# Kernel tuning notes

Hardware: AMD Instinct MI355X
Metric: run time of the kernel (lower is better)

The kernel has to match this reference:

```python
import jax, jax.numpy as jnp
import numpy as np

D, NH, NL, NP, DFF = 256, 8, 4, 4, 1024
DH = D // NH
# 4-level FPN of a 1024x1024 image at strides 8/16/32/64 (H, W per level)
SHAPES = np.array([[128, 128], [64, 64], [32, 32], [16, 16]], dtype=np.int32)


def setup_inputs() -> dict:
    ks = jax.random.split(jax.random.key(0), 16)
    B, Lq = 4, 900
    sizes = SHAPES[:, 0] * SHAPES[:, 1]
    Lin = int(sizes.sum())
    starts = np.concatenate([[0], np.cumsum(sizes)[:-1]]).astype(np.int32)
    s = 0.02  # small init so softmax/LN stay well-conditioned

    def w(k, shape):
        return jax.random.normal(k, shape, jnp.float32) * s

    return {
        "tgt": jax.random.normal(ks[0], (Lq, B, D), jnp.float32),
        "tgt_reference_points": jax.random.uniform(ks[1], (Lq, B, NL, 2), jnp.float32),
        "memory": jax.random.normal(ks[2], (Lin, B, D), jnp.float32),
        "W_off": w(ks[3], (NH * NL * NP * 2, D)), "b_off": w(ks[4], (NH * NL * NP * 2,)),
        "W_attn": w(ks[5], (NH * NL * NP, D)), "b_attn": w(ks[6], (NH * NL * NP,)),
        "W_val": w(ks[7], (D, D)), "b_val": w(ks[8], (D,)),
        "W_out": w(ks[9], (D, D)), "b_out": w(ks[10], (D,)),
        "ln1_g": jnp.ones((D,), jnp.float32), "ln1_b": jnp.zeros((D,), jnp.float32),
        "W1": w(ks[11], (DFF, D)), "b1": w(ks[12], (DFF,)),
        "W2": w(ks[13], (D, DFF)), "b2": w(ks[14], (D,)),
        "ln3_g": jnp.ones((D,), jnp.float32), "ln3_b": jnp.zeros((D,), jnp.float32),
        "memory_spatial_shapes": jnp.asarray(SHAPES),
        "memory_level_start_index": jnp.asarray(starts),
        "memory_key_padding_mask": jnp.zeros((B, Lin), jnp.bool_),
    }


def _ln(x, g, b, eps=1e-5):
    mu = x.mean(-1, keepdims=True)
    var = ((x - mu) ** 2).mean(-1, keepdims=True)
    return (x - mu) * jax.lax.rsqrt(var + eps) * g + b


def _bilinear(vl, loc, H, W):
    # vl: (B, NH, H*W, DH); loc: (B, Lq, NH, NP, 2) normalized to [0,1]
    # matches torch grid_sample(mode='bilinear', padding_mode='zeros', align_corners=False)
    B, Lq, nh, P, _ = loc.shape
    x = loc[..., 0] * W - 0.5
    y = loc[..., 1] * H - 0.5
    x0f = jnp.floor(x)
    y0f = jnp.floor(y)
    x0 = x0f.astype(jnp.int32)
    y0 = y0f.astype(jnp.int32)
    wx1 = x - x0f
    wy1 = y - y0f

    def tap(xi, yi, w):
        valid = (xi >= 0) & (xi < W) & (yi >= 0) & (yi < H)
        idx = jnp.clip(yi, 0, H - 1) * W + jnp.clip(xi, 0, W - 1)
        idx = idx.transpose(0, 2, 1, 3).reshape(B, nh, Lq * P)
        ww = (w * valid).transpose(0, 2, 1, 3).reshape(B, nh, Lq * P)
        vals = jnp.take_along_axis(vl, idx[..., None], axis=2)  # (B,NH,Lq*P,DH)
        return vals * ww[..., None]

    acc = (tap(x0, y0, (1 - wx1) * (1 - wy1)) + tap(x0 + 1, y0, wx1 * (1 - wy1))
           + tap(x0, y0 + 1, (1 - wx1) * wy1) + tap(x0 + 1, y0 + 1, wx1 * wy1))
    return acc.reshape(B, nh, Lq, P, DH)


def _msda(q, ref, value, shapes_np, W_off, b_off, W_attn, b_attn, W_out, b_out):
    # q: (B,Lq,D), ref: (B,Lq,NL,2), value: (B,Lin,NH,DH)
    B, Lq, _ = q.shape
    off = (q @ W_off.T + b_off).reshape(B, Lq, NH, NL, NP, 2)
    a = jax.nn.softmax((q @ W_attn.T + b_attn).reshape(B, Lq, NH, NL * NP), axis=-1)
    a = a.reshape(B, Lq, NH, NL, NP)
    norm = jnp.asarray(shapes_np[:, ::-1].copy(), jnp.float32)  # (NL, 2) as (W, H)
    loc = ref[:, :, None, :, None, :] + off / norm[None, None, None, :, None, :]
    sizes = [int(h) * int(w) for h, w in shapes_np]
    starts = np.concatenate([[0], np.cumsum(sizes)[:-1]])
    v = value.transpose(0, 2, 1, 3)  # (B, NH, Lin, DH)
    out = jnp.zeros((B, NH, Lq, DH), q.dtype)
    for l, (H, W) in enumerate(shapes_np):
        vl = v[:, :, int(starts[l]):int(starts[l]) + sizes[l], :]
        sampled = _bilinear(vl, loc[:, :, :, l], int(H), int(W))  # (B,NH,Lq,NP,DH)
        wl = a[:, :, :, l].transpose(0, 2, 1, 3)  # (B,NH,Lq,NP)
        out = out + (sampled * wl[..., None]).sum(3)
    out = out.transpose(0, 2, 1, 3).reshape(B, Lq, D)
    return out @ W_out.T + b_out


def reference(tgt, tgt_reference_points, memory, W_off, b_off, W_attn, b_attn,
              W_val, b_val, W_out, b_out, ln1_g, ln1_b, W1, b1, W2, b2, ln3_g, ln3_b,
              memory_spatial_shapes, memory_level_start_index, memory_key_padding_mask):
    shapes_np = np.asarray(memory_spatial_shapes)  # static level metadata
    q = tgt.transpose(1, 0, 2)                      # (B, Lq, D)
    ref = tgt_reference_points.transpose(1, 0, 2, 3)
    mem = memory.transpose(1, 0, 2)                 # (B, Lin, D)
    B, Lin, _ = mem.shape
    value = mem @ W_val.T + b_val
    value = jnp.where(memory_key_padding_mask[..., None], 0.0, value)
    value = value.reshape(B, Lin, NH, DH)
    ca = _msda(q, ref, value, shapes_np, W_off, b_off, W_attn, b_attn, W_out, b_out)
    # residual + LN (dropout is identity in eval)
    t = _ln(tgt + ca.transpose(1, 0, 2), ln1_g, ln1_b)
    # FFN
    t2 = jax.nn.relu(t @ W1.T + b1) @ W2.T + b2
    return _ln(t + t2, ln3_g, ln3_b)
```

## Files before the change

kernel.cpp:

```cpp
#include <hip/hip_runtime.h>
#include <hip/hip_bf16.h>

#define B_   4
#define LQ_  900
#define D_   256
#define NH_  8
#define DH_  32
#define NL_  4
#define NP_  4
#define DFF_ 1024
#define LIN_ 21760
#define MQ_  (LQ_*B_)
#define MV_  (LIN_*B_)
#define VALBLKS (MV_/32)

typedef __attribute__((ext_vector_type(8))) short bh8;
typedef __attribute__((ext_vector_type(4))) float f32x4;

__device__ __forceinline__ short bf16b(float f) {
    __hip_bfloat16 h = __float2bfloat16(f);
    return *reinterpret_cast<short*>(&h);
}

__device__ __forceinline__ void gload_lds16(const void* g, void* l) {
    __builtin_amdgcn_global_load_lds(
        (const __attribute__((address_space(1))) unsigned int*)g,
        (__attribute__((address_space(3))) unsigned int*)l, 16, 0, 0);
}

__device__ __forceinline__ bh8 af_from_f32(const float* p) {
    float4 v0 = *reinterpret_cast<const float4*>(p);
    float4 v1 = *reinterpret_cast<const float4*>(p + 4);
    return (bh8){ bf16b(v0.x), bf16b(v0.y), bf16b(v0.z), bf16b(v0.w),
                  bf16b(v1.x), bf16b(v1.y), bf16b(v1.z), bf16b(v1.w) };
}

__global__ __launch_bounds__(256)
void wprep_k(const float* __restrict__ Woff, const float* __restrict__ Wattn,
             const float* __restrict__ Wout, const float* __restrict__ W1,
             const float* __restrict__ W2, const float* __restrict__ Wval,
             unsigned char* __restrict__ qkvimg, unsigned char* __restrict__ outimg,
             unsigned char* __restrict__ w1img, unsigned char* __restrict__ w2img,
             unsigned char* __restrict__ valimg)
{
    const int cid = blockIdx.x*256 + threadIdx.x;
    const float* W; unsigned char* img; int KQ, c;
    if      (cid < 8192)  { W=Woff;  img=qkvimg;           KQ=8;  c=cid;       }
    else if (cid < 12288) { W=Wattn; img=qkvimg + 131072;  KQ=8;  c=cid-8192;  }
    else if (cid < 20480) { W=Wout;  img=outimg;           KQ=8;  c=cid-12288; }
    else if (cid < 53248) { W=W1;    img=w1img;            KQ=8;  c=cid-20480; }
    else if (cid < 86016) { W=W2;    img=w2img;            KQ=32; c=cid-53248; }
    else                  { W=Wval;  img=valimg;           KQ=8;  c=cid-86016; }
    const int K   = KQ*32;
    const int n16 = c & 15, g = (c>>4)&3, t = c>>6;
    const int kq  = t & (KQ-1);
    const int ntile = t >> ((KQ==8) ? 3 : 5);
    const int n = ntile*16 + n16, k0 = kq*32 + g*8;
    float4 v0 = *reinterpret_cast<const float4*>(&W[(size_t)n*K + k0]);
    float4 v1 = *reinterpret_cast<const float4*>(&W[(size_t)n*K + k0 + 4]);
    union { short s[8]; uint4 u; } pk;
    pk.s[0]=bf16b(v0.x); pk.s[1]=bf16b(v0.y); pk.s[2]=bf16b(v0.z); pk.s[3]=bf16b(v0.w);
    pk.s[4]=bf16b(v1.x); pk.s[5]=bf16b(v1.y); pk.s[6]=bf16b(v1.z); pk.s[7]=bf16b(v1.w);
    *reinterpret_cast<uint4*>(img + (size_t)(ntile*KQ + kq)*1024 + (g*16+n16)*16) = pk.u;
}

__global__ __launch_bounds__(256, 4)
void valqkv_k(const float* __restrict__ A, const unsigned char* __restrict__ Wimg,
              const float* __restrict__ bias, unsigned short* __restrict__ C,
              const unsigned char* __restrict__ mask,
              const float* __restrict__ tgt, const unsigned char* __restrict__ Qimg,
              const float* __restrict__ b_off, const float* __restrict__ b_attn,
              float* __restrict__ Yoff, float* __restrict__ Yattn)
{
    __shared__ __align__(16) unsigned char Al[32768];

    const int tid  = threadIdx.x;
    const int lane = tid & 63;

    if (blockIdx.x < VALBLKS) {
        const int wc   = tid >> 6;
        const int m0   = blockIdx.x * 32;
        const int r16  = lane & 15;
        const int g    = lane >> 4;

        const unsigned char* Abyte = (const unsigned char*)A;
        const unsigned char* wlane = Wimg + lane*16;

        const int a_row = (tid >> 3) & 31;
        const int a_x   = (tid & 7) * 16;
        const size_t a_src_row = (size_t)(m0 + a_row) * 1024 + (a_x ^ ((a_row & 7) << 4));
        const int a_dst = tid * 16;

#define ISSUE_A(KQ) gload_lds16(Abyte + a_src_row + (KQ)*128, (char*)Al + (KQ)*4096 + a_dst)
#define ISSUE_W(KQ, SLOT)                                                              \
    do { _Pragma("unroll")                                                             \
        for (int i_ = 0; i_ < 4; ++i_)                                                 \
            bfr[SLOT][i_] = *reinterpret_cast<const bh8*>(                             \
                wlane + (size_t)((wc*4 + i_)*8 + (KQ))*1024);                          \
    } while (0)

        bh8 bfr[3][4];

        ISSUE_A(0);
        ISSUE_W(0, 0);
        ISSUE_W(1, 1);
        ISSUE_A(1);
        ISSUE_A(2);

        f32x4 acc[2][4];
        #pragma unroll
        for (int i = 0; i < 2; ++i)
            #pragma unroll
            for (int j = 0; j < 4; ++j) acc[i][j] = (f32x4){0.f,0.f,0.f,0.f};

        #pragma unroll
        for (int kq = 0; kq < 8; ++kq) {
            if (kq < 6)      asm volatile("s_waitcnt vmcnt(6)" ::: "memory");
            else if (kq == 6) asm volatile("s_waitcnt vmcnt(5)" ::: "memory");
            else              asm volatile("s_waitcnt vmcnt(0)" ::: "memory");
            __builtin_amdgcn_s_barrier();

            bh8 af[2];
            #pragma unroll
            for (int mf = 0; mf < 2; ++mf) {
                const int row = mf*16 + r16;
                const int swz = (row & 7) << 4;
                const char* base = (const char*)Al + kq*4096 + row*128;
                float4 v0 = *reinterpret_cast<const float4*>(base + ((g*32     ) ^ swz));
                float4 v1 = *reinterpret_cast<const float4*>(base + ((g*32 + 16) ^ swz));
                af[mf] = (bh8){ bf16b(v0.x), bf16b(v0.y), bf16b(v0.z), bf16b(v0.w),
                                bf16b(v1.x), bf16b(v1.y), bf16b(v1.z), bf16b(v1.w) };
            }

            if (kq == 0) { ISSUE_W(2, 2); ISSUE_A(3); }
            if (kq == 1) { ISSUE_W(3, 0); ISSUE_A(4); }
            if (kq == 2) { ISSUE_W(4, 1); ISSUE_A(5); }
            if (kq == 3) { ISSUE_W(5, 2); ISSUE_A(6); }
            if (kq == 4) { ISSUE_W(6, 0); ISSUE_A(7); }
            if (kq == 5) { ISSUE_W(7, 1); }

            #pragma unroll
            for (int mf = 0; mf < 2; ++mf)
                #pragma unroll
                for (int i = 0; i < 4; ++i)
                    acc[mf][i] = __builtin_amdgcn_mfma_f32_16x16x32_bf16(af[mf], bfr[kq % 3][i], acc[mf][i], 0, 0, 0);
        }
#undef ISSUE_A
#undef ISSUE_W

        float bv[4];
        #pragma unroll
        for (int i = 0; i < 4; ++i) bv[i] = bias[wc*64 + i*16 + r16];

        #pragma unroll
        for (int mf = 0; mf < 2; ++mf) {
            #pragma unroll
            for (int r = 0; r < 4; ++r) {
                const int gm = m0 + mf*16 + g*4 + r;
                const bool z = mask[(gm & 3)*LIN_ + (gm >> 2)] != 0;
                #pragma unroll
                for (int i = 0; i < 4; ++i) {
                    float v = acc[mf][i][r] + bv[i];
                    if (z) v = 0.f;
                    C[(size_t)gm*256 + wc*64 + i*16 + r16] = (unsigned short)bf16b(v);
                }
            }
        }
    } else {
        const int w   = tid >> 6;
        const int m16 = lane & 15, g = lane >> 4;
        const int m0  = (blockIdx.x - VALBLKS) * 16;

        bh8 af[8];
        #pragma unroll
        for (int kq = 0; kq < 8; ++kq)
            af[kq] = af_from_f32(&tgt[(size_t)(m0 + m16)*256 + kq*32 + g*8]);

        f32x4 acc[6];
        #pragma unroll
        for (int i = 0; i < 6; ++i) acc[i] = (f32x4){0.f,0.f,0.f,0.f};

        #pragma unroll
        for (int i = 0; i < 6; ++i) {
            const int nt = w*6 + i;
            #pragma unroll
            for (int kq = 0; kq < 8; ++kq) {
                bh8 bf = *reinterpret_cast<const bh8*>(Qimg + (size_t)(nt*8 + kq)*1024 + lane*16);
                acc[i] = __builtin_amdgcn_mfma_f32_16x16x32_bf16(af[kq], bf, acc[i], 0, 0, 0);
            }
        }

        #pragma unroll
        for (int i = 0; i < 6; ++i) {
            const int nt = w*6 + i;
            const int j  = nt*16 + m16;
            #pragma unroll
            for (int r = 0; r < 4; ++r) {
                const int m = m0 + g*4 + r;
                if (nt < 16) Yoff[(size_t)m*256 + j] = acc[i][r] + b_off[j];
                else         Yattn[(size_t)m*128 + (j-256)] = acc[i][r] + b_attn[j-256];
            }
        }
    }
}

__global__ __launch_bounds__(1024, 2)
void outffn_k(const float* __restrict__ Amsda, const unsigned char* __restrict__ Oimg,
              const float* __restrict__ b_out, const float* __restrict__ res,
              const float* __restrict__ l1g, const float* __restrict__ l1b,
              const unsigned char* __restrict__ W1img, const float* __restrict__ b1,
              const unsigned char* __restrict__ W2img, const float* __restrict__ b2,
              const float* __restrict__ l3g, const float* __restrict__ l3b,
              float* __restrict__ Yout)
{
    __shared__ float sln[16][256];
    __shared__ __align__(16) short hl[2][16*272];

    const int tid = threadIdx.x, lane = tid & 63, w = tid >> 6;
    const int m16 = lane & 15, g = lane >> 4;
    const int m0 = blockIdx.x * 16;

    {
        bh8 af[8];
        #pragma unroll
        for (int kq = 0; kq < 8; ++kq)
            af[kq] = af_from_f32(&Amsda[(size_t)(m0 + m16)*256 + kq*32 + g*8]);

        f32x4 acc = (f32x4){0.f,0.f,0.f,0.f};
        #pragma unroll
        for (int kq = 0; kq < 8; ++kq) {
            bh8 bf = *reinterpret_cast<const bh8*>(Oimg + (size_t)(w*8 + kq)*1024 + lane*16);
            acc = __builtin_amdgcn_mfma_f32_16x16x32_bf16(af[kq], bf, acc, 0, 0, 0);
        }

        const int j = w*16 + m16;
        #pragma unroll
        for (int r = 0; r < 4; ++r) {
            const int ml = g*4 + r;
            sln[ml][j] = acc[r] + b_out[j] + res[(size_t)(m0 + ml)*256 + j];
        }
    }
    __syncthreads();

    {
        const int row = w, l2 = lane;
        float v[4], s1 = 0.f, s2 = 0.f;
        #pragma unroll
        for (int c = 0; c < 4; ++c) {
            v[c] = sln[row][l2 + c*64];
            s1 += v[c]; s2 += v[c]*v[c];
        }
        #pragma unroll
        for (int o = 32; o >= 1; o >>= 1) {
            s1 += __shfl_xor(s1, o, 64);
            s2 += __shfl_xor(s2, o, 64);
        }
        const float mu  = s1 * (1.f/256.f);
        const float var = s2 * (1.f/256.f) - mu*mu;
        const float is  = rsqrtf(var + 1e-5f);
        #pragma unroll
        for (int c = 0; c < 4; ++c) {
            const int jj = l2 + c*64;
            sln[row][jj] = (v[c] - mu) * is * l1g[jj] + l1b[jj];
        }
    }
    __syncthreads();

    bh8 af1[8];
    #pragma unroll
    for (int kq = 0; kq < 8; ++kq)
        af1[kq] = af_from_f32(&sln[m16][kq*32 + g*8]);

    f32x4 yacc = (f32x4){0.f,0.f,0.f,0.f};

    int buf = 0;
    #pragma unroll
    for (int fc = 0; fc < 4; ++fc) {
        const int ftile_g = fc*16 + w;
        f32x4 hacc = (f32x4){0.f,0.f,0.f,0.f};
        #pragma unroll
        for (int kq = 0; kq < 8; ++kq) {
            bh8 bf = *reinterpret_cast<const bh8*>(W1img + (size_t)(ftile_g*8 + kq)*1024 + lane*16);
            hacc = __builtin_amdgcn_mfma_f32_16x16x32_bf16(af1[kq], bf, hacc, 0, 0, 0);
        }
        const float bb = b1[ftile_g*16 + m16];
        #pragma unroll
        for (int r = 0; r < 4; ++r) {
            const float v = fmaxf(hacc[r] + bb, 0.f);
            hl[buf][(g*4 + r)*272 + w*16 + m16] = bf16b(v);
        }
        __syncthreads();
        bh8 a2[8];
        #pragma unroll
        for (int kqf = 0; kqf < 8; ++kqf)
            a2[kqf] = *reinterpret_cast<const bh8*>((const char*)&hl[buf][0]
                + m16*544 + (kqf*32 + g*8)*2);
        #pragma unroll
        for (int kqf = 0; kqf < 8; ++kqf) {
            const int kq2 = fc*8 + kqf;
            bh8 bf = *reinterpret_cast<const bh8*>(W2img + (size_t)(w*32 + kq2)*1024 + lane*16);
            yacc = __builtin_amdgcn_mfma_f32_16x16x32_bf16(a2[kqf], bf, yacc, 0, 0, 0);
        }
        buf ^= 1;
    }

    {
        const int j = w*16 + m16;
        #pragma unroll
        for (int r = 0; r < 4; ++r) {
            const int ml = g*4 + r;
            sln[ml][j] = yacc[r] + b2[j] + sln[ml][j];
        }
    }
    __syncthreads();

    {
        const int row = w, l2 = lane;
        float v[4], s1 = 0.f, s2 = 0.f;
        #pragma unroll
        for (int c = 0; c < 4; ++c) {
            v[c] = sln[row][l2 + c*64];
            s1 += v[c]; s2 += v[c]*v[c];
        }
        #pragma unroll
        for (int o = 32; o >= 1; o >>= 1) {
            s1 += __shfl_xor(s1, o, 64);
            s2 += __shfl_xor(s2, o, 64);
        }
        const float mu  = s1 * (1.f/256.f);
        const float var = s2 * (1.f/256.f) - mu*mu;
        const float is  = rsqrtf(var + 1e-5f);
        #pragma unroll
        for (int c = 0; c < 4; ++c) {
            const int jj = l2 + c*64;
            Yout[(size_t)(m0 + row)*256 + jj] = (v[c] - mu) * is * l3g[jj] + l3b[jj];
        }
    }
}

__global__ __launch_bounds__(256)
void msda_k(const float* __restrict__ off,
            const float* __restrict__ attnlog,
            const float* __restrict__ refp,
            const __hip_bfloat16* __restrict__ value,
            float* __restrict__ out)
{
    const int hp = threadIdx.x >> 7;
    const int dd = threadIdx.x & 127;
    const int d0 = dd * 2;
    const int m  = blockIdx.x*2 + hp;
    const int b  = m & 3;
    const int h  = dd >> 4;

    __shared__ float s_off[2][256];
    __shared__ float s_al[2][128];
    __shared__ float s_ref[2][NL_*2];
    {
        const int t2 = threadIdx.x & 127;
        s_off[hp][t2]       = off[(size_t)m*256 + t2];
        s_off[hp][t2 + 128] = off[(size_t)m*256 + t2 + 128];
        if (t2 < 128) s_al[hp][t2] = attnlog[(size_t)m*128 + t2];
        if (t2 < NL_*2) s_ref[hp][t2] = refp[(size_t)m*(NL_*2) + t2];
    }
    __syncthreads();

    float mx = -1e30f;
    #pragma unroll
    for (int t = 0; t < 16; ++t) mx = fmaxf(mx, s_al[hp][h*16 + t]);
    float e[16], ssum = 0.f;
    #pragma unroll
    for (int t = 0; t < 16; ++t) { e[t] = __expf(s_al[hp][h*16 + t] - mx); ssum += e[t]; }
    const float inv = 1.f / ssum;

    const int HS[4] = {128, 64, 32, 16};
    const int ST[4] = {0, 16384, 20480, 21504};

    float acc0 = 0.f, acc1 = 0.f;
    #pragma unroll
    for (int l = 0; l < NL_; ++l) {
        const int H = HS[l], W = HS[l], st = ST[l];
        const float rx = s_ref[hp][l*2+0], ry = s_ref[hp][l*2+1];
        #pragma unroll
        for (int p = 0; p < NP_; ++p) {
            const int base = ((h*NL_ + l)*NP_ + p);
            const float a  = e[l*4 + p] * inv;
            const float ox = s_off[hp][base*2+0], oy = s_off[hp][base*2+1];
            const float x = rx*(float)W + ox - 0.5f;
            const float y = ry*(float)H + oy - 0.5f;
            const float x0f = floorf(x), y0f = floorf(y);
            const int x0 = (int)x0f, y0 = (int)y0f;
            const float wx1 = x - x0f, wy1 = y - y0f;
            const float wx0 = 1.f - wx1, wy0 = 1.f - wy1;
            #pragma unroll
            for (int t = 0; t < 4; ++t) {
                const int xi = x0 + (t & 1);
                const int yi = y0 + (t >> 1);
                const float wgt = (t==0 ? wx0*wy0 : t==1 ? wx1*wy0 : t==2 ? wx0*wy1 : wx1*wy1);
                if (xi >= 0 && xi < W && yi >= 0 && yi < H) {
                    const size_t idx = (size_t)(st + yi*W + xi);
                    const unsigned int v = *reinterpret_cast<const unsigned int*>(
                        &value[(idx*B_ + b)*D_ + d0]);
                    const float f0 = __uint_as_float(v << 16);
                    const float f1 = __uint_as_float(v & 0xffff0000u);
                    const float aw = a * wgt;
                    acc0 = fmaf(aw, f0, acc0);
                    acc1 = fmaf(aw, f1, acc1);
                }
            }
        }
    }
    float2 o2 = { acc0, acc1 };
    *reinterpret_cast<float2*>(&out[(size_t)m*256 + d0]) = o2;
}

extern "C" void kernel_launch(void* const* d_in, const int* in_sizes, int n_in,
                              void* d_out, int out_size, void* d_ws, size_t ws_size,
                              hipStream_t stream)
{
    const float* tgt    = (const float*)d_in[0];
    const float* refp   = (const float*)d_in[1];
    const float* mem    = (const float*)d_in[2];
    const float* W_off  = (const float*)d_in[3];
    const float* b_off  = (const float*)d_in[4];
    const float* W_attn = (const float*)d_in[5];
    const float* b_attn = (const float*)d_in[6];
    const float* W_val  = (const float*)d_in[7];
    const float* b_val  = (const float*)d_in[8];
    const float* W_out  = (const float*)d_in[9];
    const float* b_out  = (const float*)d_in[10];
    const float* ln1g   = (const float*)d_in[11];
    const float* ln1b   = (const float*)d_in[12];
    const float* W1     = (const float*)d_in[13];
    const float* b1     = (const float*)d_in[14];
    const float* W2     = (const float*)d_in[15];
    const float* b2     = (const float*)d_in[16];
    const float* ln3g   = (const float*)d_in[17];
    const float* ln3b   = (const float*)d_in[18];
    const unsigned char* mask = (const unsigned char*)d_in[21];
    float* out = (float*)d_out;

    char* p = (char*)d_ws;
    __hip_bfloat16* value = (__hip_bfloat16*)p; p += (size_t)MV_*D_*2;
    float* offb = (float*)p; p += (size_t)MQ_*256*4;
    float* attl = (float*)p; p += (size_t)MQ_*128*4;
    float* msda = (float*)p; p += (size_t)MQ_*256*4;
    unsigned char* qkvimg = (unsigned char*)p; p += 196608;
    unsigned char* outimg = (unsigned char*)p; p += 131072;
    unsigned char* w1img  = (unsigned char*)p; p += 524288;
    unsigned char* w2img  = (unsigned char*)p; p += 524288;
    unsigned char* valimg = (unsigned char*)p; p += 131072;
    (void)ws_size; (void)in_sizes; (void)n_in; (void)out_size;

    wprep_k<<<dim3(368), dim3(256), 0, stream>>>(W_off, W_attn, W_out, W1, W2, W_val,
                                                 qkvimg, outimg, w1img, w2img, valimg);
    valqkv_k<<<dim3(VALBLKS + MQ_/16), dim3(256), 0, stream>>>(
        mem, valimg, b_val, (unsigned short*)value, mask,
        tgt, qkvimg, b_off, b_attn, offb, attl);
    msda_k<<<dim3(MQ_/2), dim3(256), 0, stream>>>(offb, attl, refp, value, msda);
    outffn_k<<<dim3(MQ_/16), dim3(1024), 0, stream>>>(
        msda, outimg, b_out, tgt, ln1g, ln1b,
        w1img, b1, w2img, b2, ln3g, ln3b, out);
}
```

Before: 99.43 us.

## Fuse deformable-attention sampling into the output-projection/FFN kernel

The separate msda kernel is removed. Its bilinear sampling now runs at the start of outffn_k, where each of the 16 waves handles one query row and writes the sampled result into shared memory, so the fp32 msda buffer no longer round-trips through global memory and one launch is dropped. The cost is that the sampling now runs on only 225 blocks of 1024 threads, each thread doing two channel pairs in sequence. This lowers parallelism and latency hiding for the gather-heavy stage, and the extra shared memory (about 50KB) may cut occupancy.

```diff
diff --git a/kernel.cpp b/kernel.cpp
--- a/kernel.cpp
+++ b/kernel.cpp
@@ -205,26 +205,107 @@
 }
 
 __global__ __launch_bounds__(1024, 2)
-void outffn_k(const float* __restrict__ Amsda, const unsigned char* __restrict__ Oimg,
-              const float* __restrict__ b_out, const float* __restrict__ res,
+void outffn_k(const float* __restrict__ off, const float* __restrict__ attnlog,
+              const float* __restrict__ refp, const __hip_bfloat16* __restrict__ value,
+              const unsigned char* __restrict__ Oimg, const float* __restrict__ b_out,
+              const float* __restrict__ res,
               const float* __restrict__ l1g, const float* __restrict__ l1b,
               const unsigned char* __restrict__ W1img, const float* __restrict__ b1,
               const unsigned char* __restrict__ W2img, const float* __restrict__ b2,
               const float* __restrict__ l3g, const float* __restrict__ l3b,
               float* __restrict__ Yout)
 {
-    __shared__ float sln[16][256];
+    __shared__ float X[16][264];
+    __shared__ float off_l[16][256];
+    __shared__ float al_l[16][128];
+    __shared__ float ref_l[16][8];
     __shared__ __align__(16) short hl[2][16*272];
 
     const int tid = threadIdx.x, lane = tid & 63, w = tid >> 6;
     const int m16 = lane & 15, g = lane >> 4;
     const int m0 = blockIdx.x * 16;
 
+    #pragma unroll
+    for (int i = 0; i < 4; ++i) {
+        const int idx = tid + i*1024;
+        off_l[idx >> 8][idx & 255] = off[(size_t)(m0 + (idx >> 8))*256 + (idx & 255)];
+    }
+    #pragma unroll
+    for (int i = 0; i < 2; ++i) {
+        const int idx = tid + i*1024;
+        al_l[idx >> 7][idx & 127] = attnlog[(size_t)(m0 + (idx >> 7))*128 + (idx & 127)];
+    }
+    if (tid < 128) ref_l[tid >> 3][tid & 7] = refp[(size_t)(m0 + (tid >> 3))*8 + (tid & 7)];
+    __syncthreads();
+
+    {
+        const int row = w;
+        const int b = (m0 + row) & 3;
+        const int HS[4] = {128, 64, 32, 16};
+        const int ST[4] = {0, 16384, 20480, 21504};
+        float r0[2], r1[2];
+        #pragma unroll
+        for (int uu = 0; uu < 2; ++uu) {
+            const int u  = lane + uu*64;
+            const int d0 = u*2;
+            const int h  = u >> 4;
+            float mx = -1e30f;
+            #pragma unroll
+            for (int t = 0; t < 16; ++t) mx = fmaxf(mx, al_l[row][h*16 + t]);
+            float e[16], ssum = 0.f;
+            #pragma unroll
+            for (int t = 0; t < 16; ++t) { e[t] = __expf(al_l[row][h*16 + t] - mx); ssum += e[t]; }
+            const float inv = 1.f / ssum;
+            float a0 = 0.f, a1 = 0.f;
+            #pragma unroll
+            for (int l = 0; l < NL_; ++l) {
+                const int H = HS[l], Wd = HS[l], st = ST[l];
+                const float rx = ref_l[row][l*2+0], ry = ref_l[row][l*2+1];
+                #pragma unroll
+                for (int p = 0; p < NP_; ++p) {
+                    const int base = ((h*NL_ + l)*NP_ + p);
+                    const float a  = e[l*4 + p] * inv;
+                    const float ox = off_l[row][base*2+0], oy = off_l[row][base*2+1];
+                    const float x = rx*(float)Wd + ox - 0.5f;
+                    const float y = ry*(float)H + oy - 0.5f;
+                    const float x0f = floorf(x), y0f = floorf(y);
+                    const int x0 = (int)x0f, y0 = (int)y0f;
+                    const float wx1 = x - x0f, wy1 = y - y0f;
+                    const float wx0 = 1.f - wx1, wy0 = 1.f - wy1;
+                    #pragma unroll
+                    for (int t = 0; t < 4; ++t) {
+                        const int xi = x0 + (t & 1);
+                        const int yi = y0 + (t >> 1);
+                        const float wgt = (t==0 ? wx0*wy0 : t==1 ? wx1*wy0 : t==2 ? wx0*wy1 : wx1*wy1);
+                        if (xi >= 0 && xi < Wd && yi >= 0 && yi < H) {
+                            const size_t idx = (size_t)(st + yi*Wd + xi);
+                            const unsigned int v = *reinterpret_cast<const unsigned int*>(
+                                &value[(idx*B_ + b)*D_ + d0]);
+                            const float f0 = __uint_as_float(v << 16);
+                            const float f1 = __uint_as_float(v & 0xffff0000u);
+                            const float aw = a * wgt;
+                            a0 = fmaf(aw, f0, a0);
+                            a1 = fmaf(aw, f1, a1);
+                        }
+                    }
+                }
+            }
+            r0[uu] = a0; r1[uu] = a1;
+        }
+        #pragma unroll
+        for (int uu = 0; uu < 2; ++uu) {
+            const int d0 = (lane + uu*64)*2;
+            X[row][d0]   = r0[uu];
+            X[row][d0+1] = r1[uu];
+        }
+    }
+    __syncthreads();
+
     {
         bh8 af[8];
         #pragma unroll
         for (int kq = 0; kq < 8; ++kq)
-            af[kq] = af_from_f32(&Amsda[(size_t)(m0 + m16)*256 + kq*32 + g*8]);
+            af[kq] = af_from_f32(&X[m16][kq*32 + g*8]);
 
         f32x4 acc = (f32x4){0.f,0.f,0.f,0.f};
         #pragma unroll
@@ -232,22 +313,22 @@
             bh8 bf = *reinterpret_cast<const bh8*>(Oimg + (size_t)(w*8 + kq)*1024 + lane*16);
             acc = __builtin_amdgcn_mfma_f32_16x16x32_bf16(af[kq], bf, acc, 0, 0, 0);
         }
+        __syncthreads();
 
         const int j = w*16 + m16;
         #pragma unroll
         for (int r = 0; r < 4; ++r) {
             const int ml = g*4 + r;
-            sln[ml][j] = acc[r] + b_out[j] + res[(size_t)(m0 + ml)*256 + j];
+            X[ml][j] = acc[r] + b_out[j] + res[(size_t)(m0 + ml)*256 + j];
         }
     }
     __syncthreads();
 
     {
-        const int row = w, l2 = lane;
         float v[4], s1 = 0.f, s2 = 0.f;
         #pragma unroll
         for (int c = 0; c < 4; ++c) {
-            v[c] = sln[row][l2 + c*64];
+            v[c] = X[w][lane + c*64];
             s1 += v[c]; s2 += v[c]*v[c];
         }
         #pragma unroll
@@ -260,8 +341,8 @@
         const float is  = rsqrtf(var + 1e-5f);
         #pragma unroll
         for (int c = 0; c < 4; ++c) {
-            const int jj = l2 + c*64;
-            sln[row][jj] = (v[c] - mu) * is * l1g[jj] + l1b[jj];
+            const int jj = lane + c*64;
+            X[w][jj] = (v[c] - mu) * is * l1g[jj] + l1b[jj];
         }
     }
     __syncthreads();
@@ -269,7 +350,7 @@
     bh8 af1[8];
     #pragma unroll
     for (int kq = 0; kq < 8; ++kq)
-        af1[kq] = af_from_f32(&sln[m16][kq*32 + g*8]);
+        af1[kq] = af_from_f32(&X[m16][kq*32 + g*8]);
 
     f32x4 yacc = (f32x4){0.f,0.f,0.f,0.f};
 
@@ -309,17 +390,16 @@
         #pragma unroll
         for (int r = 0; r < 4; ++r) {
             const int ml = g*4 + r;
-            sln[ml][j] = yacc[r] + b2[j] + sln[ml][j];
+            X[ml][j] = yacc[r] + b2[j] + X[ml][j];
         }
     }
     __syncthreads();
 
     {
-        const int row = w, l2 = lane;
         float v[4], s1 = 0.f, s2 = 0.f;
         #pragma unroll
         for (int c = 0; c < 4; ++c) {
-            v[c] = sln[row][l2 + c*64];
+            v[c] = X[w][lane + c*64];
             s1 += v[c]; s2 += v[c]*v[c];
         }
         #pragma unroll
@@ -332,85 +412,10 @@
         const float is  = rsqrtf(var + 1e-5f);
         #pragma unroll
         for (int c = 0; c < 4; ++c) {
-            const int jj = l2 + c*64;
-            Yout[(size_t)(m0 + row)*256 + jj] = (v[c] - mu) * is * l3g[jj] + l3b[jj];
-        }
-    }
-}
-
-__global__ __launch_bounds__(256)
-void msda_k(const float* __restrict__ off,
-            const float* __restrict__ attnlog,
-            const float* __restrict__ refp,
-            const __hip_bfloat16* __restrict__ value,
-            float* __restrict__ out)
-{
-    const int hp = threadIdx.x >> 7;
-    const int dd = threadIdx.x & 127;
-    const int d0 = dd * 2;
-    const int m  = blockIdx.x*2 + hp;
-    const int b  = m & 3;
-    const int h  = dd >> 4;
-
-    __shared__ float s_off[2][256];
-    __shared__ float s_al[2][128];
-    __shared__ float s_ref[2][NL_*2];
-    {
-        const int t2 = threadIdx.x & 127;
-        s_off[hp][t2]       = off[(size_t)m*256 + t2];
-        s_off[hp][t2 + 128] = off[(size_t)m*256 + t2 + 128];
-        if (t2 < 128) s_al[hp][t2] = attnlog[(size_t)m*128 + t2];
-        if (t2 < NL_*2) s_ref[hp][t2] = refp[(size_t)m*(NL_*2) + t2];
-    }
-    __syncthreads();
-
-    float mx = -1e30f;
-    #pragma unroll
-    for (int t = 0; t < 16; ++t) mx = fmaxf(mx, s_al[hp][h*16 + t]);
-    float e[16], ssum = 0.f;
-    #pragma unroll
-    for (int t = 0; t < 16; ++t) { e[t] = __expf(s_al[hp][h*16 + t] - mx); ssum += e[t]; }
-    const float inv = 1.f / ssum;
-
-    const int HS[4] = {128, 64, 32, 16};
-    const int ST[4] = {0, 16384, 20480, 21504};
-
-    float acc0 = 0.f, acc1 = 0.f;
-    #pragma unroll
-    for (int l = 0; l < NL_; ++l) {
-        const int H = HS[l], W = HS[l], st = ST[l];
-        const float rx = s_ref[hp][l*2+0], ry = s_ref[hp][l*2+1];
-        #pragma unroll
-        for (int p = 0; p < NP_; ++p) {
-            const int base = ((h*NL_ + l)*NP_ + p);
-            const float a  = e[l*4 + p] * inv;
-            const float ox = s_off[hp][base*2+0], oy = s_off[hp][base*2+1];
-            const float x = rx*(float)W + ox - 0.5f;
-            const float y = ry*(float)H + oy - 0.5f;
-            const float x0f = floorf(x), y0f = floorf(y);
-            const int x0 = (int)x0f, y0 = (int)y0f;
-            const float wx1 = x - x0f, wy1 = y - y0f;
-            const float wx0 = 1.f - wx1, wy0 = 1.f - wy1;
-            #pragma unroll
-            for (int t = 0; t < 4; ++t) {
-                const int xi = x0 + (t & 1);
-                const int yi = y0 + (t >> 1);
-                const float wgt = (t==0 ? wx0*wy0 : t==1 ? wx1*wy0 : t==2 ? wx0*wy1 : wx1*wy1);
-                if (xi >= 0 && xi < W && yi >= 0 && yi < H) {
-                    const size_t idx = (size_t)(st + yi*W + xi);
-                    const unsigned int v = *reinterpret_cast<const unsigned int*>(
-                        &value[(idx*B_ + b)*D_ + d0]);
-                    const float f0 = __uint_as_float(v << 16);
-                    const float f1 = __uint_as_float(v & 0xffff0000u);
-                    const float aw = a * wgt;
-                    acc0 = fmaf(aw, f0, acc0);
-                    acc1 = fmaf(aw, f1, acc1);
-                }
-            }
-        }
-    }
-    float2 o2 = { acc0, acc1 };
-    *reinterpret_cast<float2*>(&out[(size_t)m*256 + d0]) = o2;
+            const int jj = lane + c*64;
+            Yout[(size_t)(m0 + w)*256 + jj] = (v[c] - mu) * is * l3g[jj] + l3b[jj];
+        }
+    }
 }
 
 extern "C" void kernel_launch(void* const* d_in, const int* in_sizes, int n_in,
@@ -443,7 +448,6 @@
     __hip_bfloat16* value = (__hip_bfloat16*)p; p += (size_t)MV_*D_*2;
     float* offb = (float*)p; p += (size_t)MQ_*256*4;
     float* attl = (float*)p; p += (size_t)MQ_*128*4;
-    float* msda = (float*)p; p += (size_t)MQ_*256*4;
     unsigned char* qkvimg = (unsigned char*)p; p += 196608;
     unsigned char* outimg = (unsigned char*)p; p += 131072;
     unsigned char* w1img  = (unsigned char*)p; p += 524288;
@@ -456,8 +460,8 @@
     valqkv_k<<<dim3(VALBLKS + MQ_/16), dim3(256), 0, stream>>>(
         mem, valimg, b_val, (unsigned short*)value, mask,
         tgt, qkvimg, b_off, b_attn, offb, attl);
-    msda_k<<<dim3(MQ_/2), dim3(256), 0, stream>>>(offb, attl, refp, value, msda);
     outffn_k<<<dim3(MQ_/16), dim3(1024), 0, stream>>>(
-        msda, outimg, b_out, tgt, ln1g, ln1b,
+        offb, attl, refp, value,
+        outimg, b_out, tgt, ln1g, ln1b,
         w1img, b1, w2img, b2, ln3g, ln3b, out);
 }
```

Result: slower. 107.0 us (+7.6%).
